# Kernel optimization log

Hardware: AMD Instinct MI355X
Metric: run time of the kernel (lower is better)

## Reference

```python
import jax, jax.numpy as jnp
import numpy as np

B, T, D, H = 256, 128, 76, 128  # batch, time, features, lstm hidden (bidirectional -> 2H states)


def setup_inputs() -> dict:
    key = jax.random.key(0)
    ks = jax.random.split(key, 30)
    u = lambda k, shape: jax.random.uniform(k, shape, jnp.float32, -0.1, 0.1)
    inp = {}
    inp['x'] = jax.random.normal(ks[0], (B, T, D), jnp.float32)
    inp['eps_z'] = jax.random.normal(ks[1], (2, B, H), jnp.float32)
    inp['eps_on'] = jax.random.normal(ks[2], (B, T, 2 * H), jnp.float32)
    # encoder/decoder bidirectional LSTM weights: [dir, 4H, in] / [dir, 4H, H] / [dir, 4H]
    inp['enc_Wih'] = u(ks[3], (2, 4 * H, D)); inp['enc_Whh'] = u(ks[4], (2, 4 * H, H)); inp['enc_b'] = u(ks[5], (2, 4 * H))
    inp['dec_Wih'] = u(ks[6], (2, 4 * H, D)); inp['dec_Whh'] = u(ks[7], (2, 4 * H, H)); inp['dec_b'] = u(ks[8], (2, 4 * H))
    inp['Wzmu'] = u(ks[9], (H, H)); inp['bzmu'] = u(ks[10], (H,))
    inp['Wzlv'] = u(ks[11], (H, H)); inp['bzlv'] = u(ks[12], (H,))
    inp['Womu'] = u(ks[13], (2 * H, 2 * H)); inp['bomu'] = u(ks[14], (2 * H,))
    inp['Wolv'] = u(ks[15], (2 * H, 2 * H)); inp['bolv'] = u(ks[16], (2 * H,))
    inp['att_v'] = u(ks[17], (2 * H,))
    inp['att_W1'] = u(ks[18], (2 * H, 2 * H)); inp['att_b1'] = u(ks[19], (2 * H,))
    inp['att_W2'] = u(ks[20], (2 * H, 2 * H)); inp['att_b2'] = u(ks[21], (2 * H,))
    inp['Wout'] = u(ks[22], (D, 4 * H)); inp['bout'] = u(ks[23], (D,))
    return inp


def lstm_cell(xt, h, c, Wih, Whh, b):
    # PyTorch gate order: i, f, g, o
    g = xt @ Wih.T + h @ Whh.T + b
    i, f, gg, o = jnp.split(g, 4, axis=-1)
    c = jax.nn.sigmoid(f) * c + jax.nn.sigmoid(i) * jnp.tanh(gg)
    h = jax.nn.sigmoid(o) * jnp.tanh(c)
    return h, c


def reference(x, eps_z, eps_on, enc_Wih, enc_Whh, enc_b, dec_Wih, dec_Whh, dec_b,
              Wzmu, bzmu, Wzlv, bzlv, Womu, bomu, Wolv, bolv,
              att_v, att_W1, att_b1, att_W2, att_b2, Wout, bout):
    Bx, Tx, Dx = x.shape
    Hx = enc_Whh.shape[-1]
    xT = jnp.swapaxes(x, 0, 1)  # [T,B,D]
    h0 = jnp.zeros((Bx, Hx), x.dtype)
    c0 = jnp.zeros((Bx, Hx), x.dtype)

    def enc_step(d):
        def step(carry, xt):
            h, c = carry
            h, c = lstm_cell(xt, h, c, enc_Wih[d], enc_Whh[d], enc_b[d])
            return (h, c), h
        return step

    (hf, _), out_f = jax.lax.scan(enc_step(0), (h0, c0), xT)
    (hb, _), out_b = jax.lax.scan(enc_step(1), (h0, c0), xT[::-1])
    on = jnp.swapaxes(jnp.concatenate([out_f, out_b[::-1]], axis=-1), 0, 1)  # [B,T,2H]
    hn = jnp.stack([hf, hb])  # [2,B,H]

    # VAE reparameterization on final hidden and on encoder outputs
    mu_z = hn @ Wzmu.T + bzmu
    logvar_z = hn @ Wzlv.T + bzlv
    z = mu_z + eps_z * jnp.exp(0.5 * logvar_z)  # [2,B,H]
    mu_on = on @ Womu.T + bomu
    logvar_on = on @ Wolv.T + bolv
    on_s = mu_on + eps_on * jnp.exp(0.5 * logvar_on)  # [B,T,2H]

    # attention key projection precomputed once (W_2(values))
    W2v = on_s @ att_W2.T + att_b2  # [B,T,2H]
    # teacher forcing (prob=1.0): step t input is zeros at t=0, x[:,t-1] after
    dec_in = jnp.concatenate([jnp.zeros((1, Bx, Dx), x.dtype), xT[:-1]], axis=0)  # [T,B,D]

    def dec_step(carry, inp_t):
        h, c = carry  # each [2,B,H]
        q = jnp.concatenate([h[0], h[1]], axis=1)  # [B,2H]
        scores = jnp.tanh((q @ att_W1.T + att_b1)[:, None, :] + W2v) @ att_v  # [B,T]
        w = jax.nn.softmax(scores, axis=1)
        # (weights.unsqueeze(2) * values).mean(dim=1) -> weighted sum / T
        ctx = jnp.einsum('bt,btd->bd', w, on_s) / Tx  # [B,2H]
        h0n, c0n = lstm_cell(inp_t, h[0], c[0], dec_Wih[0], dec_Whh[0], dec_b[0])
        h1n, c1n = lstm_cell(inp_t, h[1], c[1], dec_Wih[1], dec_Whh[1], dec_b[1])
        out = jnp.concatenate([h0n, h1n, ctx], axis=1) @ Wout.T + bout  # [B,D]
        return (jnp.stack([h0n, h1n]), jnp.stack([c0n, c1n])), out

    _, outs = jax.lax.scan(dec_step, (z, jnp.zeros((2, Bx, Hx), x.dtype)), dec_in)
    return jnp.swapaxes(outs, 0, 1)  # [B,T,D] reconstruction
```

## Files before the change

kernel.cpp:

```cpp
#include <hip/hip_runtime.h>
#include <hip/hip_fp16.h>

#define B 256
#define T 128
#define D 76
#define H 128
#define G 512
#define H2 256

typedef unsigned int uint32;
typedef unsigned short ushort16;
typedef _Float16 h2_t __attribute__((ext_vector_type(2)));
typedef _Float16 f16x8 __attribute__((ext_vector_type(8)));
typedef float f32x4 __attribute__((ext_vector_type(4)));

__device__ __forceinline__ float sigm(float x){ return 1.0f/(1.0f+__expf(-x)); }
__device__ __forceinline__ float fast_rcp(float x){ float r; asm volatile("v_rcp_f32 %0, %1" : "=v"(r) : "v"(x)); return r; }
__device__ __forceinline__ float fast_tanh(float x){ return 1.0f - 2.0f*fast_rcp(1.0f + __expf(2.0f*x)); }
__device__ __forceinline__ uint32 pk_f16(float a, float b){
  return (uint32)__half_as_ushort(__float2half(a)) | ((uint32)__half_as_ushort(__float2half(b))<<16);
}
__device__ __forceinline__ float dot2(uint32 w, uint32 h, float acc){
  return __builtin_amdgcn_fdot2(__builtin_bit_cast(h2_t, w), __builtin_bit_cast(h2_t, h), acc, false);
}
__device__ __forceinline__ f32x4 mfma16(uint4 a, uint4 b, f32x4 c){
  return __builtin_amdgcn_mfma_f32_16x16x32_f16(
    __builtin_bit_cast(f16x8, a), __builtin_bit_cast(f16x8, b), c, 0, 0, 0);
}

struct PrepArgs {
  const float* src[2];
  float* dst[2];
  int R[2]; int C[2];
};
__global__ __launch_bounds__(256) void prep_k(PrepArgs a){
  int seg = blockIdx.x >> 5;
  const float* s=a.src[seg]; float* d=a.dst[seg];
  int R=a.R[seg], C=a.C[seg], tot=R*C;
  for (int i=(blockIdx.x&31)*256+threadIdx.x; i<tot; i+=32*256){
    int r=i/C, c=i-r*C;
    d[(size_t)c*R + r] = s[i];
  }
}

struct Pack2Args { const float* src[9]; uint32* dst[9]; int N[9]; int NP[9]; int K[9]; int KP2[9]; };
__global__ __launch_bounds__(256) void pack2_k(Pack2Args a){
  int seg = blockIdx.x >> 5;
  const float* s=a.src[seg]; uint32* d=a.dst[seg];
  int N=a.N[seg], NP=a.NP[seg], K=a.K[seg], KP2=a.KP2[seg];
  int tot=NP*KP2;
  for (int i=(blockIdx.x&31)*256+threadIdx.x; i<tot; i+=32*256){
    int k2=i/NP, j=i-k2*NP;
    uint32 v = 0;
    if (j < N && 2*k2 < K){
      float2 w = *(const float2*)(s + (size_t)j*K + 2*k2);
      v = pk_f16(w.x, w.y);
    }
    d[(size_t)k2*NP + j] = v;
  }
}

__global__ __launch_bounds__(256) void pack_whh_k(
  const float* __restrict__ eWhh, const float* __restrict__ dWhh,
  uint32* __restrict__ wpkE, uint32* __restrict__ wpkD)
{
  int idx = blockIdx.x*256 + threadIdx.x;
  int phase = idx >> 16;
  int rem = idx & 65535;
  int d = rem >> 15;
  int k2 = (rem >> 9) & 63;
  int jc = rem & 511;
  int gate = (jc>>4)&3;
  int cell = (jc&15) + 16*(jc>>6);
  int jsrc = gate*128 + cell;
  const float* Wsrc = phase ? dWhh : eWhh;
  float2 wa = *(const float2*)(Wsrc + ((size_t)(d*512 + jsrc))*128 + 2*k2);
  (phase ? wpkD : wpkE)[rem] = pk_f16(wa.x, wa.y);
}

__global__ __launch_bounds__(256) void xg_k(
  const float* __restrict__ x, const uint32* __restrict__ wx, const float* __restrict__ bias,
  uint32* __restrict__ xgp, int shift)
{
  int m0 = blockIdx.x*32;
  int d = m0 >> 15;
  int rem = m0 & 32767;
  int b = rem >> 7, t0 = rem & 127;
  int tid = threadIdx.x;
  int wv = tid>>6, lane = tid&63;
  int n0 = wv*128;
  int lr = lane & 15, kq = lane >> 4;
  __shared__ __align__(16) uint32 xs[32][48];
  for (int i=tid;i<32*48;i+=256){
    int r=i/48, k2=i-r*48, ts=t0+r-shift;
    float2 xv = (k2<38 && ts>=0) ? *(const float2*)(x + ((size_t)b*T+ts)*D + 2*k2)
                                 : make_float2(0.f,0.f);
    xs[r][k2] = pk_f16(xv.x, xv.y);
  }
  __syncthreads();
  const uint32* W = wx + (size_t)d*48*512;
  f32x4 acc[2][8];
  #pragma unroll
  for (int mt=0;mt<2;mt++)
    #pragma unroll
    for (int nt=0;nt<8;nt++) acc[mt][nt]=(f32x4){0,0,0,0};
  #pragma unroll
  for (int kb=0;kb<3;kb++){
    int k2b = kb*16 + kq*4;
    uint4 a0 = *(const uint4*)&xs[lr][k2b];
    uint4 a1 = *(const uint4*)&xs[16+lr][k2b];
    #pragma unroll
    for (int nt=0;nt<8;nt++){
      int n = n0 + nt*16 + lr;
      uint4 bw;
      bw.x = W[(size_t)(k2b+0)*512 + n]; bw.y = W[(size_t)(k2b+1)*512 + n];
      bw.z = W[(size_t)(k2b+2)*512 + n]; bw.w = W[(size_t)(k2b+3)*512 + n];
      acc[0][nt] = mfma16(a0, bw, acc[0][nt]);
      acc[1][nt] = mfma16(a1, bw, acc[1][nt]);
    }
  }
  #pragma unroll
  for (int mt=0;mt<2;mt++){
    #pragma unroll
    for (int nt=0;nt<8;nt++){
      int col = n0 + nt*16 + lr;
      float bb = bias[d*G + col];
      #pragma unroll
      for (int r=0;r<4;r++){
        int rl = mt*16 + kq*4 + r;
        float v = acc[mt][nt][r] + bb;
        float nb = __shfl_xor(v, 1);
        if ((lr&1)==0)
          xgp[((size_t)(m0+rl)*512 + col)>>1] = pk_f16(v, nb);
      }
    }
  }
}

template<int ENC>
__global__ __launch_bounds__(512,2) void rec_k(
  const __half* __restrict__ xgh, const uint32* __restrict__ wpk,
  const __half* __restrict__ h16r, __half* __restrict__ on16,
  float* __restrict__ h_fin, uint32* __restrict__ h16w)
{
  int d = blockIdx.x >> 8;
  int b = blockIdx.x & 255;
  int tid = threadIdx.x;
  int lane = tid & 63;
  int gate = lane >> 4;
  int cell = (lane & 15) + 16*(tid >> 6);
  int jmap = gate*128 + cell;
  __shared__ __align__(16) __half hsd[2][H];
  uint32 wreg[64];
  const uint32* wp = wpk + (size_t)d*64*512;
  #pragma unroll
  for (int k2=0;k2<64;k2++) wreg[k2] = wp[k2*512 + tid];
  if (tid < H){
    if (ENC) hsd[0][tid] = __float2half(0.f);
    else     hsd[0][tid] = h16r[((size_t)d*B + b)*H + tid];
  }
  float creg = 0.f, hlast = 0.f;
  const __half* xrow = xgh + (size_t)(d*B + b)*T*512;
  int te0 = ENC ? (d ? (T-1) : 0) : 0;
  __half xr_next = xrow[(size_t)te0*512 + jmap];
  __syncthreads();
  int p = 0;
  for (int t=0;t<T;t++){
    int te = ENC ? (d ? (T-1-t) : t) : t;
    __half xr = xr_next;
    if (t+1 < T){
      int tn = ENC ? (d ? (T-2-t) : (t+1)) : (t+1);
      xr_next = xrow[(size_t)tn*512 + jmap];
    }
    const uint4* h128 = (const uint4*)hsd[p];
    float acc0 = 0.f, acc1 = 0.f;
    #pragma unroll
    for (int k8=0;k8<16;k8++){
      uint4 hv4 = h128[k8];
      acc0 = dot2(wreg[4*k8+0], hv4.x, acc0);
      acc1 = dot2(wreg[4*k8+1], hv4.y, acc1);
      acc0 = dot2(wreg[4*k8+2], hv4.z, acc0);
      acc1 = dot2(wreg[4*k8+3], hv4.w, acc1);
    }
    float gpre = acc0 + acc1 + __half2float(xr);
    float kmul = (gate==2) ? 2.f : 1.f;
    float s = sigm(kmul*gpre);
    float act = (gate==2) ? fmaf(2.f, s, -1.f) : s;
    int src = lane & 15;
    float f_ = __shfl(act, src+16, 64);
    float g_ = __shfl(act, src+32, 64);
    float o_ = __shfl(act, src+48, 64);
    if (gate==0){
      creg = f_*creg + act*g_;
      float hv = o_*fast_tanh(creg);
      hlast = hv;
      hsd[p^1][cell] = __float2half(hv);
      if (ENC){
        on16[((size_t)b*T + te)*H2 + d*H + cell] = __float2half(hv);
      } else {
        float nb = __shfl_xor(hv, 1);
        if ((cell&1)==0)
          h16w[(((size_t)(t+1)*2 + d)*B + b)*64 + (cell>>1)] = pk_f16(hv, nb);
      }
    }
    __syncthreads();
    p ^= 1;
  }
  if (ENC && gate==0) h_fin[(size_t)d*B*H + (size_t)b*H + cell] = hlast;
}

__global__ __launch_bounds__(128) void z_k(
  const float* __restrict__ h_fin, const float* __restrict__ WzmuT, const float* __restrict__ bzmu,
  const float* __restrict__ WzlvT, const float* __restrict__ bzlv, const float* __restrict__ eps_z,
  uint32* __restrict__ h16w)
{
  __shared__ float hr[H];
  int d = blockIdx.x >> 8; int b = blockIdx.x & 255;
  int j = threadIdx.x;
  hr[j] = h_fin[(size_t)d*B*H + (size_t)b*H + j];
  __syncthreads();
  float mu=bzmu[j], lv=bzlv[j];
  #pragma unroll 4
  for(int k=0;k<H;k++){ float hv=hr[k]; mu+=hv*WzmuT[k*H+j]; lv+=hv*WzlvT[k*H+j]; }
  float z = mu + eps_z[(size_t)d*B*H + (size_t)b*H + j]*__expf(0.5f*lv);
  float nb = __shfl_xor(z, 1);
  if ((j&1)==0)
    h16w[(((size_t)0*2 + d)*B + b)*64 + (j>>1)] = pk_f16(z, nb);
}

__global__ __launch_bounds__(256) void onsw2v_k(
  const uint32* __restrict__ on32, const uint32* __restrict__ wpmu, const float* __restrict__ bomu,
  const uint32* __restrict__ wplv, const float* __restrict__ bolv, const float* __restrict__ eps_on,
  const uint32* __restrict__ wp2, const float* __restrict__ b2,
  uint32* __restrict__ onsT, float* __restrict__ ebg)
{
  __shared__ __align__(16) uint32 tl[32][128];
  __shared__ __align__(16) uint32 t2p[32][128];
  size_t row0=(size_t)blockIdx.x*32;
  int b = (int)(row0 >> 7), t0 = (int)(row0 & 127);
  int tid=threadIdx.x;
  int wv = tid>>6, lane = tid&63;
  int n0 = wv*64;
  int lr = lane & 15, kq = lane >> 4;
  for(int i=tid;i<32*128;i+=256) ((uint32*)tl)[i] = on32[row0*128 + i];
  __syncthreads();
  f32x4 accM[2][4], accL[2][4];
  #pragma unroll
  for (int mt=0;mt<2;mt++)
    #pragma unroll
    for (int nt=0;nt<4;nt++){ accM[mt][nt]=(f32x4){0,0,0,0}; accL[mt][nt]=(f32x4){0,0,0,0}; }
  for (int kb=0;kb<8;kb++){
    int k2b = kb*16 + kq*4;
    uint4 aA0 = *(const uint4*)&tl[lr][k2b];
    uint4 aA1 = *(const uint4*)&tl[16+lr][k2b];
    #pragma unroll
    for (int nt=0;nt<4;nt++){
      int n = n0 + nt*16 + lr;
      uint4 bM, bL;
      bM.x = wpmu[(size_t)(k2b+0)*H2 + n]; bM.y = wpmu[(size_t)(k2b+1)*H2 + n];
      bM.z = wpmu[(size_t)(k2b+2)*H2 + n]; bM.w = wpmu[(size_t)(k2b+3)*H2 + n];
      bL.x = wplv[(size_t)(k2b+0)*H2 + n]; bL.y = wplv[(size_t)(k2b+1)*H2 + n];
      bL.z = wplv[(size_t)(k2b+2)*H2 + n]; bL.w = wplv[(size_t)(k2b+3)*H2 + n];
      accM[0][nt] = mfma16(aA0, bM, accM[0][nt]);
      accM[1][nt] = mfma16(aA1, bM, accM[1][nt]);
      accL[0][nt] = mfma16(aA0, bL, accL[0][nt]);
      accL[1][nt] = mfma16(aA1, bL, accL[1][nt]);
    }
  }
  #pragma unroll
  for (int mt=0;mt<2;mt++){
    #pragma unroll
    for (int nt=0;nt<4;nt++){
      int col = n0 + nt*16 + lr;
      float bm = bomu[col], bl = bolv[col];
      #pragma unroll
      for (int r=0;r<4;r++){
        int rl = mt*16 + kq*4 + r;
        size_t rowg = row0 + rl;
        float mu = accM[mt][nt][r] + bm;
        float lv = accL[mt][nt][r] + bl;
        float v = mu + eps_on[rowg*H2 + col]*__expf(0.5f*lv);
        float nb = __shfl_xor(v, 1);
        if ((lr&1)==0) t2p[rl][col>>1] = pk_f16(v, nb);
      }
    }
  }
  __syncthreads();
  #pragma unroll
  for(int rr=0;rr<16;rr++){
    uint32 ua = t2p[2*rr][tid>>1], ub = t2p[2*rr+1][tid>>1];
    uint32 ha = (tid&1) ? (ua>>16) : (ua & 0xffffu);
    uint32 hb = (tid&1) ? (ub>>16) : (ub & 0xffffu);
    onsT[((size_t)b*H2 + tid)*64 + (t0>>1) + rr] = ha | (hb<<16);
  }
  f32x4 acc3[2][4];
  #pragma unroll
  for (int mt=0;mt<2;mt++)
    #pragma unroll
    for (int nt=0;nt<4;nt++) acc3[mt][nt]=(f32x4){0,0,0,0};
  for (int kb=0;kb<8;kb++){
    int k2b = kb*16 + kq*4;
    uint4 aA0 = *(const uint4*)&t2p[lr][k2b];
    uint4 aA1 = *(const uint4*)&t2p[16+lr][k2b];
    #pragma unroll
    for (int nt=0;nt<4;nt++){
      int n = n0 + nt*16 + lr;
      uint4 bW;
      bW.x = wp2[(size_t)(k2b+0)*H2 + n]; bW.y = wp2[(size_t)(k2b+1)*H2 + n];
      bW.z = wp2[(size_t)(k2b+2)*H2 + n]; bW.w = wp2[(size_t)(k2b+3)*H2 + n];
      acc3[0][nt] = mfma16(aA0, bW, acc3[0][nt]);
      acc3[1][nt] = mfma16(aA1, bW, acc3[1][nt]);
    }
  }
  #pragma unroll
  for (int mt=0;mt<2;mt++){
    #pragma unroll
    for (int nt=0;nt<4;nt++){
      int col = n0 + nt*16 + lr;
      float bb = b2[col];
      #pragma unroll
      for (int r=0;r<4;r++){
        int rl = mt*16 + kq*4 + r;
        ebg[(row0 + rl)*H2 + col] = __expf(2.0f*(acc3[mt][nt][r] + bb));
      }
    }
  }
}

__global__ __launch_bounds__(256) void qp_all_k(
  const uint32* __restrict__ h16, const uint32* __restrict__ wp1, const float* __restrict__ b1,
  float* __restrict__ eqg)
{
  int m0 = blockIdx.x*32; int b = m0>>7; int t0 = m0&127;
  __shared__ __align__(16) uint32 tile[32][128];
  int tid=threadIdx.x;
  int wv = tid>>6, lane = tid&63;
  int n0 = wv*64;
  int lr = lane & 15, kq = lane >> 4;
  for (int i=tid;i<32*128;i+=256){
    int r=i>>7, c=i&127; int dd=c>>6, kk2=c&63;
    tile[r][c] = h16[(((size_t)(t0+r)*2 + dd)*B + b)*64 + kk2];
  }
  __syncthreads();
  f32x4 acc[2][4];
  #pragma unroll
  for (int mt=0;mt<2;mt++)
    #pragma unroll
    for (int nt=0;nt<4;nt++) acc[mt][nt]=(f32x4){0,0,0,0};
  for (int kb=0;kb<8;kb++){
    int k2b = kb*16 + kq*4;
    uint4 aA0 = *(const uint4*)&tile[lr][k2b];
    uint4 aA1 = *(const uint4*)&tile[16+lr][k2b];
    #pragma unroll
    for (int nt=0;nt<4;nt++){
      int n = n0 + nt*16 + lr;
      uint4 bW;
      bW.x = wp1[(size_t)(k2b+0)*H2 + n]; bW.y = wp1[(size_t)(k2b+1)*H2 + n];
      bW.z = wp1[(size_t)(k2b+2)*H2 + n]; bW.w = wp1[(size_t)(k2b+3)*H2 + n];
      acc[0][nt] = mfma16(aA0, bW, acc[0][nt]);
      acc[1][nt] = mfma16(aA1, bW, acc[1][nt]);
    }
  }
  #pragma unroll
  for (int mt=0;mt<2;mt++){
    #pragma unroll
    for (int nt=0;nt<4;nt++){
      int col = n0 + nt*16 + lr;
      float bb = b1[col];
      #pragma unroll
      for (int r=0;r<4;r++){
        int rl = mt*16 + kq*4 + r;
        eqg[(size_t)(m0 + rl)*H2 + col] = __expf(2.0f*(acc[mt][nt][r] + bb));
      }
    }
  }
}

__global__ __launch_bounds__(512,2) void score_k(
  const float* __restrict__ eqg, const float* __restrict__ ebg,
  const float* __restrict__ att_v, uint32* __restrict__ sc16)
{
  int b  = blockIdx.x >> 1;
  int t0 = (blockIdx.x & 1) * 64;
  int tid = threadIdx.x;
  int jq = tid & 15, ttb = tid >> 4;
  __shared__ __align__(16) float eqs[2][4*320];
  __shared__ __align__(16) float scl[2][4][T];
  __shared__ float wsum8[2][8];
  __shared__ __align__(16) float wvsp[320];
  float eb0[16], eb1[16], eb2[16], eb3[16];
  float vsum_mine = 0.f;
  {
    const float* ebb = ebg + (size_t)b*T*H2;
    #pragma unroll
    for (int ii=0;ii<16;ii++){
      int j = 16*jq + ii;
      eb0[ii] = ebb[(size_t)(ttb    )*H2 + j];
      eb1[ii] = ebb[(size_t)(ttb+32 )*H2 + j];
      eb2[ii] = ebb[(size_t)(ttb+64 )*H2 + j];
      eb3[ii] = ebb[(size_t)(ttb+96 )*H2 + j];
      vsum_mine += att_v[j];
    }
  }
  if (tid < H2) wvsp[(tid>>4)*20 + (tid&15)] = -2.0f*att_v[tid];
  if (tid < 256){
    int q = tid>>6, l = 4*(tid&63);
    float4 v = ((const float4*)(eqg + ((size_t)b*T + t0 + q)*H2))[tid&63];
    *(float4*)&eqs[0][q*320 + (l>>4)*20 + (l&15)] = v;
  }
  __syncthreads();
  int buf = 0;
  for (int tq=0; tq<64; tq+=4){
    int cur = (tq>>2)&1;
    if (tq+4 < 64 && tid < 256){
      int q = tid>>6, l = 4*(tid&63);
      float4 v = ((const float4*)(eqg + ((size_t)b*T + t0+tq+4 + q)*H2))[tid&63];
      *(float4*)&eqs[buf^1][q*320 + (l>>4)*20 + (l&15)] = v;
    }
    const float* eqb = eqs[buf];
    float a00=vsum_mine,a01=vsum_mine,a02=vsum_mine,a03=vsum_mine;
    float a10=vsum_mine,a11=vsum_mine,a12=vsum_mine,a13=vsum_mine;
    float a20=vsum_mine,a21=vsum_mine,a22=vsum_mine,a23=vsum_mine;
    float a30=vsum_mine,a31=vsum_mine,a32=vsum_mine,a33=vsum_mine;
    #pragma unroll
    for (int ii4=0; ii4<4; ii4++){
      float4 q0 = *(const float4*)&eqb[        jq*20 + 4*ii4];
      float4 q1 = *(const float4*)&eqb[320   + jq*20 + 4*ii4];
      float4 q2 = *(const float4*)&eqb[2*320 + jq*20 + 4*ii4];
      float4 q3 = *(const float4*)&eqb[3*320 + jq*20 + 4*ii4];
      float4 w4 = *(const float4*)&wvsp[jq*20 + 4*ii4];
      #pragma unroll
      for (int c=0;c<4;c++){
        int ii = 4*ii4 + c;
        float e0=eb0[ii], e1=eb1[ii], e2=eb2[ii], e3=eb3[ii];
        float q0c = (c==0)?q0.x:(c==1)?q0.y:(c==2)?q0.z:q0.w;
        float q1c = (c==0)?q1.x:(c==1)?q1.y:(c==2)?q1.z:q1.w;
        float q2c = (c==0)?q2.x:(c==1)?q2.y:(c==2)?q2.z:q2.w;
        float q3c = (c==0)?q3.x:(c==1)?q3.y:(c==2)?q3.z:q3.w;
        float w   = (c==0)?w4.x:(c==1)?w4.y:(c==2)?w4.z:w4.w;
        a00 = fmaf(w, fast_rcp(fmaf(e0,q0c,1.f)), a00);
        a01 = fmaf(w, fast_rcp(fmaf(e1,q0c,1.f)), a01);
        a02 = fmaf(w, fast_rcp(fmaf(e2,q0c,1.f)), a02);
        a03 = fmaf(w, fast_rcp(fmaf(e3,q0c,1.f)), a03);
        a10 = fmaf(w, fast_rcp(fmaf(e0,q1c,1.f)), a10);
        a11 = fmaf(w, fast_rcp(fmaf(e1,q1c,1.f)), a11);
        a12 = fmaf(w, fast_rcp(fmaf(e2,q1c,1.f)), a12);
        a13 = fmaf(w, fast_rcp(fmaf(e3,q1c,1.f)), a13);
        a20 = fmaf(w, fast_rcp(fmaf(e0,q2c,1.f)), a20);
        a21 = fmaf(w, fast_rcp(fmaf(e1,q2c,1.f)), a21);
        a22 = fmaf(w, fast_rcp(fmaf(e2,q2c,1.f)), a22);
        a23 = fmaf(w, fast_rcp(fmaf(e3,q2c,1.f)), a23);
        a30 = fmaf(w, fast_rcp(fmaf(e0,q3c,1.f)), a30);
        a31 = fmaf(w, fast_rcp(fmaf(e1,q3c,1.f)), a31);
        a32 = fmaf(w, fast_rcp(fmaf(e2,q3c,1.f)), a32);
        a33 = fmaf(w, fast_rcp(fmaf(e3,q3c,1.f)), a33);
      }
    }
    #pragma unroll
    for (int off=1; off<16; off<<=1){
      a00 += __shfl_xor(a00,off); a01 += __shfl_xor(a01,off);
      a02 += __shfl_xor(a02,off); a03 += __shfl_xor(a03,off);
      a10 += __shfl_xor(a10,off); a11 += __shfl_xor(a11,off);
      a12 += __shfl_xor(a12,off); a13 += __shfl_xor(a13,off);
      a20 += __shfl_xor(a20,off); a21 += __shfl_xor(a21,off);
      a22 += __shfl_xor(a22,off); a23 += __shfl_xor(a23,off);
      a30 += __shfl_xor(a30,off); a31 += __shfl_xor(a31,off);
      a32 += __shfl_xor(a32,off); a33 += __shfl_xor(a33,off);
    }
    if (jq==0){
      scl[cur][0][ttb]=__expf(a00); scl[cur][0][ttb+32]=__expf(a01);
      scl[cur][0][ttb+64]=__expf(a02); scl[cur][0][ttb+96]=__expf(a03);
      scl[cur][1][ttb]=__expf(a10); scl[cur][1][ttb+32]=__expf(a11);
      scl[cur][1][ttb+64]=__expf(a12); scl[cur][1][ttb+96]=__expf(a13);
      scl[cur][2][ttb]=__expf(a20); scl[cur][2][ttb+32]=__expf(a21);
      scl[cur][2][ttb+64]=__expf(a22); scl[cur][2][ttb+96]=__expf(a23);
      scl[cur][3][ttb]=__expf(a30); scl[cur][3][ttb+32]=__expf(a31);
      scl[cur][3][ttb+64]=__expf(a32); scl[cur][3][ttb+96]=__expf(a33);
    }
    __syncthreads();
    {
      int row = tid>>7;
      float e = scl[cur][row][tid&127];
      #pragma unroll
      for (int off=1; off<64; off<<=1) e += __shfl_xor(e,off);
      if ((tid&63)==0) wsum8[cur][tid>>6]=e;
    }
    __syncthreads();
    if (tid < 256){
      int row = tid>>6, i = tid&63;
      float tot = wsum8[cur][row*2] + wsum8[cur][row*2+1];
      float inv = fast_rcp(tot*128.0f);
      sc16[((size_t)b*T + t0+tq+row)*64 + i] =
        pk_f16(scl[cur][row][2*i]*inv, scl[cur][row][2*i+1]*inv);
    }
    buf ^= 1;
  }
}

__global__ __launch_bounds__(256,2) void pvout_k(
  const uint32* __restrict__ sc16, const uint32* __restrict__ onsT,
  const uint32* __restrict__ h16, const uint32* __restrict__ wpout,
  const float* __restrict__ bout, float* __restrict__ out)
{
  int b  = blockIdx.x >> 3;
  int t0 = (blockIdx.x & 7) * 16;
  int m0 = blockIdx.x*16;
  int tid = threadIdx.x;
  int wv = tid>>6, lane = tid&63;
  int lr = lane & 15, kq = lane >> 4;
  __shared__ __align__(16) uint32 scs[16][64];
  __shared__ __align__(16) uint32 rb[16][256];
  for (int i=tid;i<1024;i+=256) ((uint32*)scs)[i] = sc16[((size_t)b*T + t0)*64 + i];
  for (int i=tid;i<16*128;i+=256){
    int r=i>>7, c=i&127;
    int t = t0+r;
    rb[r][c] = (c<64) ? h16[(((size_t)(t+1)*2 + 0)*B + b)*64 + c]
                      : h16[(((size_t)(t+1)*2 + 1)*B + b)*64 + (c-64)];
  }
  __syncthreads();
  {
    int n0 = wv*64;
    f32x4 accP[4];
    #pragma unroll
    for (int nt=0;nt<4;nt++) accP[nt]=(f32x4){0,0,0,0};
    #pragma unroll
    for (int kb=0;kb<4;kb++){
      int k2b = kb*16 + kq*4;
      uint4 a = *(const uint4*)&scs[lr][k2b];
      #pragma unroll
      for (int nt=0;nt<4;nt++){
        int j = n0 + nt*16 + lr;
        uint4 bw = *(const uint4*)(onsT + ((size_t)b*H2 + j)*64 + k2b);
        accP[nt] = mfma16(a, bw, accP[nt]);
      }
    }
    #pragma unroll
    for (int nt=0;nt<4;nt++){
      int j = n0 + nt*16 + lr;
      #pragma unroll
      for (int r=0;r<4;r++){
        int row = kq*4 + r;
        float v = accP[nt][r];
        float nb = __shfl_xor(v, 1);
        if ((lr&1)==0) rb[row][128 + (j>>1)] = pk_f16(v, nb);
      }
    }
  }
  __syncthreads();
  for (int tt=wv; tt<5; tt+=4){
    f32x4 acc = (f32x4){0,0,0,0};
    #pragma unroll
    for (int kb=0;kb<16;kb++){
      int k2b = kb*16 + kq*4;
      uint4 a = *(const uint4*)&rb[lr][k2b];
      uint4 bw;
      bw.x = wpout[(size_t)(k2b+0)*80 + tt*16+lr]; bw.y = wpout[(size_t)(k2b+1)*80 + tt*16+lr];
      bw.z = wpout[(size_t)(k2b+2)*80 + tt*16+lr]; bw.w = wpout[(size_t)(k2b+3)*80 + tt*16+lr];
      acc = mfma16(a, bw, acc);
    }
    int col = tt*16 + lr;
    if (col < D){
      float bb = bout[col];
      #pragma unroll
      for (int r=0;r<4;r++)
        out[(size_t)(m0 + kq*4 + r)*D + col] = acc[r] + bb;
    }
  }
}

extern "C" void kernel_launch(void* const* d_in, const int* in_sizes, int n_in,
                              void* d_out, int out_size, void* d_ws, size_t ws_size,
                              hipStream_t stream) {
  const float* x      =(const float*)d_in[0];
  const float* eps_z  =(const float*)d_in[1];
  const float* eps_on =(const float*)d_in[2];
  const float* enc_Wih=(const float*)d_in[3];
  const float* enc_Whh=(const float*)d_in[4];
  const float* enc_b  =(const float*)d_in[5];
  const float* dec_Wih=(const float*)d_in[6];
  const float* dec_Whh=(const float*)d_in[7];
  const float* dec_b  =(const float*)d_in[8];
  const float* Wzmu=(const float*)d_in[9];  const float* bzmu=(const float*)d_in[10];
  const float* Wzlv=(const float*)d_in[11]; const float* bzlv=(const float*)d_in[12];
  const float* Womu=(const float*)d_in[13]; const float* bomu=(const float*)d_in[14];
  const float* Wolv=(const float*)d_in[15]; const float* bolv=(const float*)d_in[16];
  const float* att_v=(const float*)d_in[17];
  const float* att_W1=(const float*)d_in[18]; const float* att_b1=(const float*)d_in[19];
  const float* att_W2=(const float*)d_in[20]; const float* att_b2=(const float*)d_in[21];
  const float* Wout=(const float*)d_in[22];  const float* bout=(const float*)d_in[23];
  float* out=(float*)d_out;
  float* ws=(float*)d_ws;
  (void)ws_size; (void)n_in; (void)in_sizes; (void)out_size;

  size_t o=0;
  float* WzmuT=ws+o; o+=H*H;
  float* WzlvT=ws+o; o+=H*H;
  uint32* wpkE=(uint32*)(ws+o); o+=65536;
  uint32* wpkD=(uint32*)(ws+o); o+=65536;
  uint32* wpmu=(uint32*)(ws+o); o+=32768;
  uint32* wplv=(uint32*)(ws+o); o+=32768;
  uint32* wp1 =(uint32*)(ws+o); o+=32768;
  uint32* wp2 =(uint32*)(ws+o); o+=32768;
  uint32* wpout=(uint32*)(ws+o); o+=20480;
  uint32* wxE =(uint32*)(ws+o); o+=49152;
  uint32* wxD =(uint32*)(ws+o); o+=49152;
  float* h_fin=ws+o; o+=2*B*H;
  __half* on16=(__half*)(ws+o); o+=(size_t)B*T*H2/2;
  uint32* h16 =(uint32*)(ws+o); o+=(size_t)(T+1)*2*B*64;
  float* Abase=ws+o; o+=16777216;
  float* Cbase=ws+o; o+=14680064;

  uint32* xgp = (uint32*)Abase;
  __half* xgh = (__half*)Abase;
  float* eqg  = Abase;
  uint32* onsT = (uint32*)Cbase;
  float* ebg  = Cbase + 4194304;
  uint32* sc16 = (uint32*)(Cbase + 4194304 + 8388608);

  PrepArgs pa;
  {
    const float* srcs[2]={Wzmu,Wzlv};
    float* dsts[2]={WzmuT,WzlvT};
    for(int i=0;i<2;i++){pa.src[i]=srcs[i];pa.dst[i]=dsts[i];pa.R[i]=H;pa.C[i]=H;}
  }
  Pack2Args p2;
  {
    const float* srcs[9]={Womu,Wolv,att_W1,att_W2,Wout,
                          enc_Wih, enc_Wih + (size_t)512*76,
                          dec_Wih, dec_Wih + (size_t)512*76};
    uint32* dsts[9]={wpmu,wplv,wp1,wp2,wpout, wxE, wxE+24576, wxD, wxD+24576};
    int Ns [9]={H2,H2,H2,H2, D, 512,512,512,512};
    int NPs[9]={H2,H2,H2,H2, 80, 512,512,512,512};
    int Ks [9]={H2,H2,H2,H2, G, D,D,D,D};
    int KP2[9]={128,128,128,128, 256, 48,48,48,48};
    for(int i=0;i<9;i++){p2.src[i]=srcs[i];p2.dst[i]=dsts[i];p2.N[i]=Ns[i];p2.NP[i]=NPs[i];p2.K[i]=Ks[i];p2.KP2[i]=KP2[i];}
  }
  prep_k<<<64,256,0,stream>>>(pa);
  pack2_k<<<288,256,0,stream>>>(p2);
  pack_whh_k<<<512,256,0,stream>>>(enc_Whh, dec_Whh, wpkE, wpkD);

  xg_k<<<2048,256,0,stream>>>(x, wxE, enc_b, xgp, 0);
  rec_k<1><<<512,512,0,stream>>>(xgh, wpkE, nullptr, on16, h_fin, nullptr);
  z_k<<<512,128,0,stream>>>(h_fin, WzmuT,bzmu,WzlvT,bzlv,eps_z, h16);
  onsw2v_k<<<1024,256,0,stream>>>((const uint32*)on16,wpmu,bomu,wplv,bolv,eps_on,wp2,att_b2,onsT,ebg);

  xg_k<<<2048,256,0,stream>>>(x, wxD, dec_b, xgp, 1);
  rec_k<0><<<512,512,0,stream>>>(xgh, wpkD, (const __half*)h16, nullptr, nullptr, h16);

  qp_all_k<<<1024,256,0,stream>>>(h16, wp1, att_b1, eqg);
  score_k<<<512,512,0,stream>>>(eqg, ebg, att_v, sc16);
  pvout_k<<<2048,256,0,stream>>>(sc16, onsT, h16, wpout, bout, out);
}
```

Measured before the change: 612.3 us.

## Batch 16 sequences per LSTM block and compute recurrence with MFMA

The recurrent kernel now handles 16 batch rows per block and computes the h·Whh product with 16x16x32 f16 MFMA, with weights held in registers as MFMA B-fragments. Before, each block ran one sequence using scalar dot2. The input-gate projection kernel now writes its output in a matching fragment-friendly layout so each lane loads its xg values as one uint4 per gate. The aim is to replace per-sequence scalar dot products and cross-lane gate shuffles with matrix-core work. In exchange the recurrence launches only 32 blocks, which may leave most CUs idle, and the per-step critical path grows with more activations per thread.

Result: slower. 867.0 us (+41.6%).

```diff
diff --git a/kernel.cpp b/kernel.cpp
--- a/kernel.cpp
+++ b/kernel.cpp
@@ -19,6 +19,9 @@
 __device__ __forceinline__ float fast_tanh(float x){ return 1.0f - 2.0f*fast_rcp(1.0f + __expf(2.0f*x)); }
 __device__ __forceinline__ uint32 pk_f16(float a, float b){
   return (uint32)__half_as_ushort(__float2half(a)) | ((uint32)__half_as_ushort(__float2half(b))<<16);
+}
+__device__ __forceinline__ float h2f_sel(uint32 u, int hi){
+  return __half2float(__ushort_as_half((unsigned short)(hi ? (u>>16) : (u & 0xffffu))));
 }
 __device__ __forceinline__ float dot2(uint32 w, uint32 h, float acc){
   return __builtin_amdgcn_fdot2(__builtin_bit_cast(h2_t, w), __builtin_bit_cast(h2_t, h), acc, false);
@@ -80,22 +83,26 @@
 
 __global__ __launch_bounds__(256) void xg_k(
   const float* __restrict__ x, const uint32* __restrict__ wx, const float* __restrict__ bias,
-  uint32* __restrict__ xgp, int shift)
-{
-  int m0 = blockIdx.x*32;
-  int d = m0 >> 15;
-  int rem = m0 & 32767;
-  int b = rem >> 7, t0 = rem & 127;
+  uint32* __restrict__ xgq, int shift)
+{
+  int bi = blockIdx.x;
+  int d  = bi >> 10;
+  int rem = bi & 1023;
+  int bg = rem >> 6;
+  int t0 = (rem & 63) * 2;
   int tid = threadIdx.x;
   int wv = tid>>6, lane = tid&63;
   int n0 = wv*128;
   int lr = lane & 15, kq = lane >> 4;
   __shared__ __align__(16) uint32 xs[32][48];
   for (int i=tid;i<32*48;i+=256){
-    int r=i/48, k2=i-r*48, ts=t0+r-shift;
+    int rl=i/48, k2=i-rl*48;
+    int tt=rl>>4, brow=rl&15;
+    int ts = t0+tt-shift;
+    int b = bg*16+brow;
     float2 xv = (k2<38 && ts>=0) ? *(const float2*)(x + ((size_t)b*T+ts)*D + 2*k2)
                                  : make_float2(0.f,0.f);
-    xs[r][k2] = pk_f16(xv.x, xv.y);
+    xs[rl][k2] = pk_f16(xv.x, xv.y);
   }
   __syncthreads();
   const uint32* W = wx + (size_t)d*48*512;
@@ -125,88 +132,117 @@
     for (int nt=0;nt<8;nt++){
       int col = n0 + nt*16 + lr;
       float bb = bias[d*G + col];
+      int gate = col >> 7, cell = col & 127;
+      int jc  = (cell>>4)*64 + gate*16 + (cell&15);
+      int jcp = jc >> 1;
+      size_t base = (((size_t)(d*16+bg)*T + (t0+mt))*256 + jcp)*16;
       #pragma unroll
       for (int r=0;r<4;r++){
-        int rl = mt*16 + kq*4 + r;
         float v = acc[mt][nt][r] + bb;
         float nb = __shfl_xor(v, 1);
         if ((lr&1)==0)
-          xgp[((size_t)(m0+rl)*512 + col)>>1] = pk_f16(v, nb);
+          xgq[base + kq*4 + r] = pk_f16(v, nb);
       }
     }
   }
 }
 
 template<int ENC>
-__global__ __launch_bounds__(512,2) void rec_k(
-  const __half* __restrict__ xgh, const uint32* __restrict__ wpk,
-  const __half* __restrict__ h16r, __half* __restrict__ on16,
+__global__ __launch_bounds__(512,1) void rec_k(
+  const uint32* __restrict__ xgq, const uint32* __restrict__ wpk,
+  const uint32* __restrict__ h16r, __half* __restrict__ on16,
   float* __restrict__ h_fin, uint32* __restrict__ h16w)
 {
-  int d = blockIdx.x >> 8;
-  int b = blockIdx.x & 255;
+  int d  = blockIdx.x >> 4;
+  int bg = blockIdx.x & 15;
   int tid = threadIdx.x;
+  int w  = tid >> 6;
   int lane = tid & 63;
-  int gate = lane >> 4;
-  int cell = (lane & 15) + 16*(tid >> 6);
-  int jmap = gate*128 + cell;
-  __shared__ __align__(16) __half hsd[2][H];
-  uint32 wreg[64];
-  const uint32* wp = wpk + (size_t)d*64*512;
-  #pragma unroll
-  for (int k2=0;k2<64;k2++) wreg[k2] = wp[k2*512 + tid];
-  if (tid < H){
-    if (ENC) hsd[0][tid] = __float2half(0.f);
-    else     hsd[0][tid] = h16r[((size_t)d*B + b)*H + tid];
-  }
-  float creg = 0.f, hlast = 0.f;
-  const __half* xrow = xgh + (size_t)(d*B + b)*T*512;
-  int te0 = ENC ? (d ? (T-1) : 0) : 0;
-  __half xr_next = xrow[(size_t)te0*512 + jmap];
-  __syncthreads();
-  int p = 0;
+  int lr = lane & 15, kq = lane >> 4;
+  int c  = w*16 + lr;
+  int hi = lr & 1;
+  __shared__ __align__(16) uint32 hbuf[2][16][64];
+  uint4 wreg[4][4];
+  {
+    const uint32* wp = wpk + (size_t)d*64*512;
+    #pragma unroll
+    for (int g=0; g<4; g++){
+      int jc = w*64 + g*16 + lr;
+      #pragma unroll
+      for (int kb=0; kb<4; kb++){
+        int k2b = kb*16 + kq*4;
+        wreg[g][kb].x = wp[(size_t)(k2b+0)*512 + jc];
+        wreg[g][kb].y = wp[(size_t)(k2b+1)*512 + jc];
+        wreg[g][kb].z = wp[(size_t)(k2b+2)*512 + jc];
+        wreg[g][kb].w = wp[(size_t)(k2b+3)*512 + jc];
+      }
+    }
+  }
+  for (int i=tid; i<16*64; i+=512){
+    int r=i>>6, c2=i&63;
+    hbuf[0][r][c2] = ENC ? 0u : h16r[(((size_t)d)*B + (bg*16+r))*64 + c2];
+  }
+  const uint32* xbase = xgq + (size_t)(d*16+bg)*T*4096;
+  int jcp[4];
+  #pragma unroll
+  for (int g=0;g<4;g++) jcp[g] = (w*64 + g*16 + lr) >> 1;
+  uint4 xg4[4];
+  {
+    int te0 = ENC ? (d ? (T-1) : 0) : 0;
+    #pragma unroll
+    for (int g=0;g<4;g++)
+      xg4[g] = *(const uint4*)(xbase + ((size_t)te0*256 + jcp[g])*16 + kq*4);
+  }
+  float creg[4] = {0,0,0,0};
+  float hlast[4] = {0,0,0,0};
+  __syncthreads();
+  int p=0;
   for (int t=0;t<T;t++){
     int te = ENC ? (d ? (T-1-t) : t) : t;
-    __half xr = xr_next;
+    f32x4 acc[4];
+    #pragma unroll
+    for (int g=0;g<4;g++) acc[g]=(f32x4){0,0,0,0};
+    #pragma unroll
+    for (int kb=0;kb<4;kb++){
+      int k2b = kb*16 + kq*4;
+      uint4 a = *(const uint4*)&hbuf[p][lr][k2b];
+      acc[0] = mfma16(a, wreg[0][kb], acc[0]);
+      acc[1] = mfma16(a, wreg[1][kb], acc[1]);
+      acc[2] = mfma16(a, wreg[2][kb], acc[2]);
+      acc[3] = mfma16(a, wreg[3][kb], acc[3]);
+    }
+    uint4 xc0=xg4[0], xc1=xg4[1], xc2=xg4[2], xc3=xg4[3];
     if (t+1 < T){
       int tn = ENC ? (d ? (T-2-t) : (t+1)) : (t+1);
-      xr_next = xrow[(size_t)tn*512 + jmap];
-    }
-    const uint4* h128 = (const uint4*)hsd[p];
-    float acc0 = 0.f, acc1 = 0.f;
-    #pragma unroll
-    for (int k8=0;k8<16;k8++){
-      uint4 hv4 = h128[k8];
-      acc0 = dot2(wreg[4*k8+0], hv4.x, acc0);
-      acc1 = dot2(wreg[4*k8+1], hv4.y, acc1);
-      acc0 = dot2(wreg[4*k8+2], hv4.z, acc0);
-      acc1 = dot2(wreg[4*k8+3], hv4.w, acc1);
-    }
-    float gpre = acc0 + acc1 + __half2float(xr);
-    float kmul = (gate==2) ? 2.f : 1.f;
-    float s = sigm(kmul*gpre);
-    float act = (gate==2) ? fmaf(2.f, s, -1.f) : s;
-    int src = lane & 15;
-    float f_ = __shfl(act, src+16, 64);
-    float g_ = __shfl(act, src+32, 64);
-    float o_ = __shfl(act, src+48, 64);
-    if (gate==0){
-      creg = f_*creg + act*g_;
-      float hv = o_*fast_tanh(creg);
-      hlast = hv;
-      hsd[p^1][cell] = __float2half(hv);
-      if (ENC){
-        on16[((size_t)b*T + te)*H2 + d*H + cell] = __float2half(hv);
-      } else {
-        float nb = __shfl_xor(hv, 1);
-        if ((cell&1)==0)
-          h16w[(((size_t)(t+1)*2 + d)*B + b)*64 + (cell>>1)] = pk_f16(hv, nb);
-      }
+      #pragma unroll
+      for (int g=0;g<4;g++)
+        xg4[g] = *(const uint4*)(xbase + ((size_t)tn*256 + jcp[g])*16 + kq*4);
+    }
+    #pragma unroll
+    for (int r=0;r<4;r++){
+      float gi = acc[0][r] + h2f_sel(((const uint32*)&xc0)[r], hi);
+      float gf = acc[1][r] + h2f_sel(((const uint32*)&xc1)[r], hi);
+      float gg = acc[2][r] + h2f_sel(((const uint32*)&xc2)[r], hi);
+      float go = acc[3][r] + h2f_sel(((const uint32*)&xc3)[r], hi);
+      float i_=sigm(gi), f_=sigm(gf), g_=fast_tanh(gg), o_=sigm(go);
+      creg[r] = f_*creg[r] + i_*g_;
+      float hv = o_*fast_tanh(creg[r]);
+      hlast[r] = hv;
+      float nb = __shfl_xor(hv, 1);
+      if (!hi) hbuf[p^1][kq*4+r][c>>1] = pk_f16(hv, nb);
+      if (ENC)
+        on16[((size_t)(bg*16+kq*4+r)*T + te)*H2 + d*H + c] = __float2half(hv);
+      else if (!hi)
+        h16w[(((size_t)(t+1)*2 + d)*B + (bg*16+kq*4+r))*64 + (c>>1)] = pk_f16(hv, nb);
     }
     __syncthreads();
     p ^= 1;
   }
-  if (ENC && gate==0) h_fin[(size_t)d*B*H + (size_t)b*H + cell] = hlast;
+  if (ENC){
+    #pragma unroll
+    for (int r=0;r<4;r++)
+      h_fin[(size_t)d*B*H + (size_t)(bg*16+kq*4+r)*H + c] = hlast[r];
+  }
 }
 
 __global__ __launch_bounds__(128) void z_k(
@@ -610,8 +646,7 @@
   float* Abase=ws+o; o+=16777216;
   float* Cbase=ws+o; o+=14680064;
 
-  uint32* xgp = (uint32*)Abase;
-  __half* xgh = (__half*)Abase;
+  uint32* xgq = (uint32*)Abase;
   float* eqg  = Abase;
   uint32* onsT = (uint32*)Cbase;
   float* ebg  = Cbase + 4194304;
@@ -639,13 +674,13 @@
   pack2_k<<<288,256,0,stream>>>(p2);
   pack_whh_k<<<512,256,0,stream>>>(enc_Whh, dec_Whh, wpkE, wpkD);
 
-  xg_k<<<2048,256,0,stream>>>(x, wxE, enc_b, xgp, 0);
-  rec_k<1><<<512,512,0,stream>>>(xgh, wpkE, nullptr, on16, h_fin, nullptr);
+  xg_k<<<2048,256,0,stream>>>(x, wxE, enc_b, xgq, 0);
+  rec_k<1><<<32,512,0,stream>>>(xgq, wpkE, nullptr, on16, h_fin, nullptr);
   z_k<<<512,128,0,stream>>>(h_fin, WzmuT,bzmu,WzlvT,bzlv,eps_z, h16);
   onsw2v_k<<<1024,256,0,stream>>>((const uint32*)on16,wpmu,bomu,wplv,bolv,eps_on,wp2,att_b2,onsT,ebg);
 
-  xg_k<<<2048,256,0,stream>>>(x, wxD, dec_b, xgp, 1);
-  rec_k<0><<<512,512,0,stream>>>(xgh, wpkD, (const __half*)h16, nullptr, nullptr, h16);
+  xg_k<<<2048,256,0,stream>>>(x, wxD, dec_b, xgq, 1);
+  rec_k<0><<<32,512,0,stream>>>(xgq, wpkD, h16, nullptr, nullptr, h16);
 
   qp_all_k<<<1024,256,0,stream>>>(h16, wp1, att_b1, eqg);
   score_k<<<512,512,0,stream>>>(eqg, ebg, att_v, sc16);
```
